# Performance work log

Measured on AMD Instinct MI355X. Metric: run time of the kernel, lower is better.

The kernel has to match this reference:

```python
import jax, jax.numpy as jnp
import numpy as np

H = 2048          # hidden_size
N = 16384         # batch (= events processed in one forward)
THR = 0.7         # event_threshold
NEG = -1e30       # masked-softmax fill


def setup_inputs() -> dict:
    key = jax.random.key(0)
    ks = jax.random.split(key, 8)
    s = lambda k, shape, scale: (jax.random.normal(k, shape, dtype=jnp.float32) * scale)
    return {
        "x": jax.random.normal(ks[0], (N, H), dtype=jnp.float32),
        "importance": jax.random.uniform(ks[1], (N,), dtype=jnp.float32),
        # event_detector: Linear(H, H//2) -> ReLU -> Linear(H//2, 1) -> Sigmoid
        "W_e1": s(ks[2], (H, H // 2), 0.02), "b_e1": jnp.zeros((H // 2,), jnp.float32),
        "W_e2": s(ks[3], (H // 2, 1), 0.05), "b_e2": jnp.ones((1,), jnp.float32),
        # retrieval_network: Linear(H, H//2) -> ReLU -> Linear(H//2, H) -> Sigmoid
        "W_r1": s(ks[4], (H, H // 2), 0.02), "b_r1": jnp.zeros((H // 2,), jnp.float32),
        "W_r2": s(ks[5], (H // 2, H), 0.02), "b_r2": jnp.zeros((H,), jnp.float32),
        "timestamp": 0,
    }


def reference(x, importance, W_e1, b_e1, W_e2, b_e2, W_r1, b_r1, W_r2, b_r2, timestamp):
    # --- detect_events: MLP -> sigmoid -> threshold -------------------------
    scores = jax.nn.sigmoid(jnp.maximum(x @ W_e1 + b_e1, 0.0) @ W_e2 + b_e2)[:, 0]  # [N]
    events = scores > THR                                   # bool mask = event-gated scatter
    has_events = jnp.any(events)

    # --- store_memory + consolidate_memories --------------------------------
    # Event rows are written into the ring buffer (no wraparound since N <= capacity);
    # consolidation = softmax over stored importances, weighted sum of stored rows.
    logits = jnp.where(events, importance, NEG)             # masked softmax over event rows
    w = jax.nn.softmax(logits)                              # [N]
    w = jnp.where(events, w, 0.0)
    consolidated = w @ x                                    # [H]

    # --- retrieve_memory -----------------------------------------------------
    # After consolidation memory_count == 1, so softmax(similarities) == 1 for
    # every query row and retrieved_memory == consolidated (broadcast to [N,H]).
    retrieved = jax.nn.sigmoid(jnp.maximum(consolidated @ W_r1 + b_r1, 0.0) @ W_r2 + b_r2)  # [H]

    # If no events fired, memory_count == 0 and retrieve_memory returns zeros.
    add = jnp.where(has_events, retrieved, jnp.zeros_like(retrieved))
    return x + add[None, :]
```

## Files before the change

### kernel.cpp

```cpp
#include <hip/hip_runtime.h>
#include <hip/hip_bf16.h>

#define H_    2048
#define NROWS 16384
#define HH    1024

typedef __bf16 bf16x8 __attribute__((ext_vector_type(8)));
typedef float  floatx4 __attribute__((ext_vector_type(4)));

__device__ __forceinline__ unsigned f2bf(float f) {
  unsigned u = __builtin_bit_cast(unsigned, f);
  u += 0x7fff + ((u >> 16) & 1);
  return u >> 16;
}

__device__ __forceinline__ void gload_lds16(const void* g, void* l) {
  __builtin_amdgcn_global_load_lds(
      (const __attribute__((address_space(1))) unsigned*)g,
      (__attribute__((address_space(3))) unsigned*)l, 16, 0, 0);
}

__global__ __launch_bounds__(256) void convert_x_kernel(
    const float* __restrict__ x, unsigned short* __restrict__ xb)
{
  size_t i = ((size_t)blockIdx.x * 256 + threadIdx.x) * 8;
  float4 v0 = *reinterpret_cast<const float4*>(x + i);
  float4 v1 = *reinterpret_cast<const float4*>(x + i + 4);
  uint4 o;
  o.x = f2bf(v0.x) | (f2bf(v0.y) << 16);
  o.y = f2bf(v0.z) | (f2bf(v0.w) << 16);
  o.z = f2bf(v1.x) | (f2bf(v1.y) << 16);
  o.w = f2bf(v1.z) | (f2bf(v1.w) << 16);
  *reinterpret_cast<uint4*>(xb + i) = o;
}

__global__ __launch_bounds__(256) void transpose_w1_kernel(
    const float* __restrict__ W1, unsigned short* __restrict__ W1t)
{
  __shared__ unsigned short tile[64][66];
  int k0 = blockIdx.x * 64;
  int n0 = blockIdx.y * 64;
  int t = threadIdx.x;
#pragma unroll
  for (int i = 0; i < 4; i++) {
    int idx = t + i * 256;
    int r = idx >> 4, c4 = (idx & 15) << 2;
    float4 v = *reinterpret_cast<const float4*>(W1 + (size_t)(k0 + r) * HH + n0 + c4);
    tile[r][c4 + 0] = (unsigned short)f2bf(v.x);
    tile[r][c4 + 1] = (unsigned short)f2bf(v.y);
    tile[r][c4 + 2] = (unsigned short)f2bf(v.z);
    tile[r][c4 + 3] = (unsigned short)f2bf(v.w);
  }
  __syncthreads();
#pragma unroll
  for (int i = 0; i < 2; i++) {
    int idx = t + i * 256;
    int n = idx >> 3, k8 = (idx & 7) << 3;
    uint4 o;
    o.x = (unsigned)tile[k8 + 0][n] | ((unsigned)tile[k8 + 1][n] << 16);
    o.y = (unsigned)tile[k8 + 2][n] | ((unsigned)tile[k8 + 3][n] << 16);
    o.z = (unsigned)tile[k8 + 4][n] | ((unsigned)tile[k8 + 5][n] << 16);
    o.w = (unsigned)tile[k8 + 6][n] | ((unsigned)tile[k8 + 7][n] << 16);
    *reinterpret_cast<uint4*>(W1t + (size_t)(n0 + n) * H_ + k0 + k8) = o;
  }
}

__global__ __launch_bounds__(256) void gemm_v2_kernel(
    const unsigned short* __restrict__ xb, const unsigned short* __restrict__ W1t,
    const float* __restrict__ b1, const float* __restrict__ W2,
    float* __restrict__ s_pre)
{
  __shared__ unsigned short As[128 * 32];
  __shared__ unsigned short Bs[128 * 32];

  const int t    = threadIdx.x;
  const int n0   = blockIdx.x * 128;
  const int m0   = blockIdx.y * 128;
  const int wave = t >> 6, lane = t & 63;
  const int wr   = (wave >> 1) * 64;
  const int wc   = (wave & 1) * 64;
  const int lcol = lane & 15, quad = lane >> 4;

  floatx4 acc[4][4] = {};

  const unsigned short* ag0 = xb  + (size_t)(m0 + (t >> 2)) * H_ + (t & 3) * 8;
  const unsigned short* ag1 = ag0 + (size_t)64 * H_;
  const unsigned short* bg0 = W1t + (size_t)(n0 + (t >> 2)) * H_ + (t & 3) * 8;
  const unsigned short* bg1 = bg0 + (size_t)64 * H_;
  unsigned short* al0 = As + 512 * wave;
  unsigned short* al1 = As + 2048 + 512 * wave;
  unsigned short* bl0 = Bs + 512 * wave;
  unsigned short* bl1 = Bs + 2048 + 512 * wave;

  for (int kk = 0; kk < H_; kk += 32) {
    __syncthreads();
    gload_lds16(ag0 + kk, al0);
    gload_lds16(ag1 + kk, al1);
    gload_lds16(bg0 + kk, bl0);
    gload_lds16(bg1 + kk, bl1);
    __syncthreads();

    bf16x8 af[4], bfr[4];
#pragma unroll
    for (int mt = 0; mt < 4; mt++)
      af[mt] = *reinterpret_cast<const bf16x8*>(As + (wr + mt * 16 + lcol) * 32 + quad * 8);
#pragma unroll
    for (int nt = 0; nt < 4; nt++)
      bfr[nt] = *reinterpret_cast<const bf16x8*>(Bs + (wc + nt * 16 + lcol) * 32 + quad * 8);
#pragma unroll
    for (int mt = 0; mt < 4; mt++)
#pragma unroll
      for (int nt = 0; nt < 4; nt++)
        acc[mt][nt] = __builtin_amdgcn_mfma_f32_16x16x32_bf16(af[mt], bfr[nt], acc[mt][nt], 0, 0, 0);
  }

  float rowsum[4][4];
#pragma unroll
  for (int mt = 0; mt < 4; mt++)
#pragma unroll
    for (int r = 0; r < 4; r++) rowsum[mt][r] = 0.f;

#pragma unroll
  for (int nt = 0; nt < 4; nt++) {
    int n = n0 + wc + nt * 16 + lcol;
    float b1v = b1[n], w2v = W2[n];
#pragma unroll
    for (int mt = 0; mt < 4; mt++)
#pragma unroll
      for (int r = 0; r < 4; r++) {
        float h = fmaxf(acc[mt][nt][r] + b1v, 0.f);
        rowsum[mt][r] = fmaf(h, w2v, rowsum[mt][r]);
      }
  }
#pragma unroll
  for (int mt = 0; mt < 4; mt++)
#pragma unroll
    for (int r = 0; r < 4; r++) {
      float s = rowsum[mt][r];
      s += __shfl_xor(s, 1); s += __shfl_xor(s, 2);
      s += __shfl_xor(s, 4); s += __shfl_xor(s, 8);
      if (lcol == 0)
        atomicAdd(&s_pre[m0 + wr + mt * 16 + quad * 4 + r], s);
    }
}

__global__ __launch_bounds__(256) void gemm_score_kernel(
    const float* __restrict__ x, const float* __restrict__ W1,
    const float* __restrict__ b1, const float* __restrict__ W2,
    float* __restrict__ s_pre)
{
  __shared__ unsigned short As[128][40];
  __shared__ unsigned short Bs[128][40];
  const int t    = threadIdx.x;
  const int n0   = blockIdx.x * 128;
  const int m0   = blockIdx.y * 128;
  const int wave = t >> 6, lane = t & 63;
  const int wr   = (wave >> 1) * 64;
  const int wc   = (wave & 1) * 64;
  const int lcol = lane & 15, quad = lane >> 4;
  floatx4 acc[4][4] = {};

  for (int kk = 0; kk < H_; kk += 32) {
    __syncthreads();
#pragma unroll
    for (int i = 0; i < 4; i++) {
      int idx = t + i * 256;
      int row = idx >> 3, k4 = (idx & 7) << 2;
      float4 v = *reinterpret_cast<const float4*>(x + (size_t)(m0 + row) * H_ + kk + k4);
      unsigned lo = f2bf(v.x) | (f2bf(v.y) << 16);
      unsigned hi = f2bf(v.z) | (f2bf(v.w) << 16);
      *reinterpret_cast<uint2*>(&As[row][k4]) = make_uint2(lo, hi);
    }
#pragma unroll
    for (int i = 0; i < 4; i++) {
      int idx = t + i * 256;
      int kr = idx >> 5, c4 = (idx & 31) << 2;
      float4 v = *reinterpret_cast<const float4*>(W1 + (size_t)(kk + kr) * HH + n0 + c4);
      Bs[c4 + 0][kr] = (unsigned short)f2bf(v.x);
      Bs[c4 + 1][kr] = (unsigned short)f2bf(v.y);
      Bs[c4 + 2][kr] = (unsigned short)f2bf(v.z);
      Bs[c4 + 3][kr] = (unsigned short)f2bf(v.w);
    }
    __syncthreads();
    bf16x8 af[4], bfr[4];
#pragma unroll
    for (int mt = 0; mt < 4; mt++)
      af[mt] = *reinterpret_cast<const bf16x8*>(&As[wr + mt * 16 + lcol][quad * 8]);
#pragma unroll
    for (int nt = 0; nt < 4; nt++)
      bfr[nt] = *reinterpret_cast<const bf16x8*>(&Bs[wc + nt * 16 + lcol][quad * 8]);
#pragma unroll
    for (int mt = 0; mt < 4; mt++)
#pragma unroll
      for (int nt = 0; nt < 4; nt++)
        acc[mt][nt] = __builtin_amdgcn_mfma_f32_16x16x32_bf16(af[mt], bfr[nt], acc[mt][nt], 0, 0, 0);
  }
  float rowsum[4][4];
#pragma unroll
  for (int mt = 0; mt < 4; mt++)
#pragma unroll
    for (int r = 0; r < 4; r++) rowsum[mt][r] = 0.f;
#pragma unroll
  for (int nt = 0; nt < 4; nt++) {
    int n = n0 + wc + nt * 16 + lcol;
    float b1v = b1[n], w2v = W2[n];
#pragma unroll
    for (int mt = 0; mt < 4; mt++)
#pragma unroll
      for (int r = 0; r < 4; r++) {
        float h = fmaxf(acc[mt][nt][r] + b1v, 0.f);
        rowsum[mt][r] = fmaf(h, w2v, rowsum[mt][r]);
      }
  }
#pragma unroll
  for (int mt = 0; mt < 4; mt++)
#pragma unroll
    for (int r = 0; r < 4; r++) {
      float s = rowsum[mt][r];
      s += __shfl_xor(s, 1); s += __shfl_xor(s, 2);
      s += __shfl_xor(s, 4); s += __shfl_xor(s, 8);
      if (lcol == 0)
        atomicAdd(&s_pre[m0 + wr + mt * 16 + quad * 4 + r], s);
    }
}

__global__ __launch_bounds__(256) void score_kernel(
    const float* __restrict__ s_pre, const float* __restrict__ imp,
    const float* __restrict__ b2, float* __restrict__ wbuf,
    float* __restrict__ Z, float* __restrict__ cnt)
{
  int i = blockIdx.x * 256 + threadIdx.x;
  float s = s_pre[i] + b2[0];
  float sig = 1.f / (1.f + __expf(-s));
  bool ev = sig > 0.7f;
  float w = ev ? __expf(imp[i]) : 0.f;
  wbuf[i] = w;
  float cw = ev ? 1.f : 0.f;
#pragma unroll
  for (int off = 32; off; off >>= 1) {
    w  += __shfl_down(w, off);
    cw += __shfl_down(cw, off);
  }
  if ((threadIdx.x & 63) == 0) {
    atomicAdd(Z, w);
    atomicAdd(cnt, cw);
  }
}

__global__ __launch_bounds__(256) void consolidate_kernel(
    const float* __restrict__ x, const float* __restrict__ wbuf,
    float* __restrict__ c)
{
  int t = threadIdx.x;
  int r0 = blockIdx.x * 128;
  float a[8] = {0.f, 0.f, 0.f, 0.f, 0.f, 0.f, 0.f, 0.f};
  for (int r = 0; r < 128; r++) {
    float w = wbuf[r0 + r];
    if (w != 0.f) {
      const float4* xr = reinterpret_cast<const float4*>(x + (size_t)(r0 + r) * H_);
      float4 v0 = xr[t], v1 = xr[t + 256];
      a[0] = fmaf(w, v0.x, a[0]); a[1] = fmaf(w, v0.y, a[1]);
      a[2] = fmaf(w, v0.z, a[2]); a[3] = fmaf(w, v0.w, a[3]);
      a[4] = fmaf(w, v1.x, a[4]); a[5] = fmaf(w, v1.y, a[5]);
      a[6] = fmaf(w, v1.z, a[6]); a[7] = fmaf(w, v1.w, a[7]);
    }
  }
  int j0 = t * 4;
  atomicAdd(&c[j0 + 0], a[0]); atomicAdd(&c[j0 + 1], a[1]);
  atomicAdd(&c[j0 + 2], a[2]); atomicAdd(&c[j0 + 3], a[3]);
  atomicAdd(&c[1024 + j0 + 0], a[4]); atomicAdd(&c[1024 + j0 + 1], a[5]);
  atomicAdd(&c[1024 + j0 + 2], a[6]); atomicAdd(&c[1024 + j0 + 3], a[7]);
}

__global__ __launch_bounds__(256) void r1_kernel(
    const float* __restrict__ c, const float* __restrict__ Z,
    const float* __restrict__ cnt, const float* __restrict__ Wr1,
    float* __restrict__ hr)
{
  __shared__ float cs[128];
  int n  = blockIdx.x * 256 + threadIdx.x;
  int k0 = blockIdx.y * 128;
  float inv = (cnt[0] > 0.5f) ? (1.f / Z[0]) : 0.f;
  if (threadIdx.x < 128) cs[threadIdx.x] = c[k0 + threadIdx.x] * inv;
  __syncthreads();
  float s = 0.f;
#pragma unroll 8
  for (int k = 0; k < 128; k++)
    s = fmaf(cs[k], Wr1[(size_t)(k0 + k) * HH + n], s);
  atomicAdd(&hr[n], s);
}

__global__ __launch_bounds__(256) void r2_kernel(
    const float* __restrict__ hr, const float* __restrict__ br1,
    const float* __restrict__ Wr2, float* __restrict__ rt)
{
  __shared__ float hs[128];
  int n  = blockIdx.x * 256 + threadIdx.x;
  int k0 = blockIdx.y * 128;
  if (threadIdx.x < 128)
    hs[threadIdx.x] = fmaxf(hr[k0 + threadIdx.x] + br1[k0 + threadIdx.x], 0.f);
  __syncthreads();
  float s = 0.f;
#pragma unroll 8
  for (int k = 0; k < 128; k++)
    s = fmaf(hs[k], Wr2[(size_t)(k0 + k) * H_ + n], s);
  atomicAdd(&rt[n], s);
}

__global__ __launch_bounds__(256) void finalize_kernel(
    const float* __restrict__ rt, const float* __restrict__ br2,
    const float* __restrict__ cnt, float* __restrict__ addv)
{
  int j = blockIdx.x * 256 + threadIdx.x;
  float v = 0.f;
  if (cnt[0] > 0.5f) v = 1.f / (1.f + expf(-(rt[j] + br2[j])));
  addv[j] = v;
}

__global__ __launch_bounds__(256) void out_kernel(
    const float* __restrict__ x, const float* __restrict__ addv,
    float* __restrict__ out)
{
  size_t i = (size_t)blockIdx.x * 256 + threadIdx.x;
  int j4 = (int)(i & 511);
  float4 a = reinterpret_cast<const float4*>(addv)[j4];
  float4 v = reinterpret_cast<const float4*>(x)[i];
  v.x += a.x; v.y += a.y; v.z += a.z; v.w += a.w;
  reinterpret_cast<float4*>(out)[i] = v;
}

extern "C" void kernel_launch(void* const* d_in, const int* in_sizes, int n_in,
                              void* d_out, int out_size, void* d_ws, size_t ws_size,
                              hipStream_t stream)
{
  (void)in_sizes; (void)n_in; (void)out_size;
  const float* x   = (const float*)d_in[0];
  const float* imp = (const float*)d_in[1];
  const float* We1 = (const float*)d_in[2];
  const float* be1 = (const float*)d_in[3];
  const float* We2 = (const float*)d_in[4];
  const float* be2 = (const float*)d_in[5];
  const float* Wr1 = (const float*)d_in[6];
  const float* br1 = (const float*)d_in[7];
  const float* Wr2 = (const float*)d_in[8];
  const float* br2 = (const float*)d_in[9];
  float* out = (float*)d_out;

  float* ws    = (float*)d_ws;
  float* s_pre = ws;
  float* c     = ws + 16384;
  float* hr    = ws + 18432;
  float* rt    = ws + 19456;
  float* Z     = ws + 21504;
  float* cnt   = ws + 21505;
  float* wbuf  = ws + 21760;
  float* addv  = ws + 38144;

  const size_t scal_bytes = 49152 * sizeof(float);
  const size_t xb_bytes   = (size_t)NROWS * H_ * 2;
  const size_t w1t_bytes  = (size_t)HH * H_ * 2;
  unsigned short* xb  = (unsigned short*)((char*)d_ws + scal_bytes);
  unsigned short* W1t = (unsigned short*)((char*)d_ws + scal_bytes + xb_bytes);
  const bool fast = ws_size >= scal_bytes + xb_bytes + w1t_bytes;

  hipMemsetAsync(d_ws, 0, 21506 * sizeof(float), stream);

  if (fast) {
    convert_x_kernel<<<16384, 256, 0, stream>>>(x, xb);
    transpose_w1_kernel<<<dim3(32, 16), 256, 0, stream>>>(We1, W1t);
    gemm_v2_kernel<<<dim3(8, 128), 256, 0, stream>>>(xb, W1t, be1, We2, s_pre);
  } else {
    gemm_score_kernel<<<dim3(8, 128), 256, 0, stream>>>(x, We1, be1, We2, s_pre);
  }
  score_kernel<<<64, 256, 0, stream>>>(s_pre, imp, be2, wbuf, Z, cnt);
  consolidate_kernel<<<128, 256, 0, stream>>>(x, wbuf, c);
  r1_kernel<<<dim3(4, 16), 256, 0, stream>>>(c, Z, cnt, Wr1, hr);
  r2_kernel<<<dim3(8, 8), 256, 0, stream>>>(hr, br1, Wr2, rt);
  finalize_kernel<<<8, 256, 0, stream>>>(rt, br2, cnt, addv);
  out_kernel<<<32768, 256, 0, stream>>>(x, addv, out);
}
```

Measured before the change: 467.8 us.

## Consolidate from bf16 copy of x, recompute weights inline, swap GEMM grid order

The consolidation pass now reads the bf16 copy of x instead of fp32, halving its memory traffic. It recomputes the event weights per block from s_pre rather than reading a stored weight buffer, and uses 512 blocks of 32 rows instead of 128 blocks of 128. The GEMM grid is transposed so consecutive blocks walk along M, which changes L2 reuse of the xb and W1t tiles. The bf16 consolidation loses precision in the weighted sum, and the old early skip of zero-weight rows is gone, so all rows are now read.

```diff
diff --git a/kernel.cpp b/kernel.cpp
--- a/kernel.cpp
+++ b/kernel.cpp
@@ -12,6 +12,12 @@
   unsigned u = __builtin_bit_cast(unsigned, f);
   u += 0x7fff + ((u >> 16) & 1);
   return u >> 16;
+}
+__device__ __forceinline__ float bflo(unsigned u) {
+  return __builtin_bit_cast(float, u << 16);
+}
+__device__ __forceinline__ float bfhi(unsigned u) {
+  return __builtin_bit_cast(float, u & 0xffff0000u);
 }
 
 __device__ __forceinline__ void gload_lds16(const void* g, void* l) {
@@ -74,8 +80,8 @@
   __shared__ unsigned short Bs[128 * 32];
 
   const int t    = threadIdx.x;
-  const int n0   = blockIdx.x * 128;
-  const int m0   = blockIdx.y * 128;
+  const int m0   = blockIdx.x * 128;
+  const int n0   = blockIdx.y * 128;
   const int wave = t >> 6, lane = t & 63;
   const int wr   = (wave >> 1) * 64;
   const int wc   = (wave & 1) * 64;
@@ -226,15 +232,13 @@
 
 __global__ __launch_bounds__(256) void score_kernel(
     const float* __restrict__ s_pre, const float* __restrict__ imp,
-    const float* __restrict__ b2, float* __restrict__ wbuf,
-    float* __restrict__ Z, float* __restrict__ cnt)
+    const float* __restrict__ b2, float* __restrict__ Z, float* __restrict__ cnt)
 {
   int i = blockIdx.x * 256 + threadIdx.x;
   float s = s_pre[i] + b2[0];
   float sig = 1.f / (1.f + __expf(-s));
   bool ev = sig > 0.7f;
   float w = ev ? __expf(imp[i]) : 0.f;
-  wbuf[i] = w;
   float cw = ev ? 1.f : 0.f;
 #pragma unroll
   for (int off = 32; off; off >>= 1) {
@@ -247,23 +251,60 @@
   }
 }
 
+__global__ __launch_bounds__(256) void consolidate_v2_kernel(
+    const unsigned short* __restrict__ xb, const float* __restrict__ s_pre,
+    const float* __restrict__ imp, const float* __restrict__ b2,
+    float* __restrict__ c)
+{
+  __shared__ float wsh[32];
+  int t = threadIdx.x;
+  int r0 = blockIdx.x * 32;
+  if (t < 32) {
+    float s = s_pre[r0 + t] + b2[0];
+    float sig = 1.f / (1.f + __expf(-s));
+    wsh[t] = (sig > 0.7f) ? __expf(imp[r0 + t]) : 0.f;
+  }
+  __syncthreads();
+  float a[8] = {0.f, 0.f, 0.f, 0.f, 0.f, 0.f, 0.f, 0.f};
+  const unsigned short* xp = xb + (size_t)r0 * H_ + t * 8;
+#pragma unroll 4
+  for (int r = 0; r < 32; r++) {
+    float w = wsh[r];
+    uint4 v = *reinterpret_cast<const uint4*>(xp + (size_t)r * H_);
+    a[0] = fmaf(w, bflo(v.x), a[0]); a[1] = fmaf(w, bfhi(v.x), a[1]);
+    a[2] = fmaf(w, bflo(v.y), a[2]); a[3] = fmaf(w, bfhi(v.y), a[3]);
+    a[4] = fmaf(w, bflo(v.z), a[4]); a[5] = fmaf(w, bfhi(v.z), a[5]);
+    a[6] = fmaf(w, bflo(v.w), a[6]); a[7] = fmaf(w, bfhi(v.w), a[7]);
+  }
+  int j0 = t * 8;
+#pragma unroll
+  for (int q = 0; q < 8; q++) atomicAdd(&c[j0 + q], a[q]);
+}
+
 __global__ __launch_bounds__(256) void consolidate_kernel(
-    const float* __restrict__ x, const float* __restrict__ wbuf,
+    const float* __restrict__ x, const float* __restrict__ s_pre,
+    const float* __restrict__ imp, const float* __restrict__ b2,
     float* __restrict__ c)
 {
+  __shared__ float wsh[32];
   int t = threadIdx.x;
-  int r0 = blockIdx.x * 128;
+  int r0 = blockIdx.x * 32;
+  if (t < 32) {
+    float s = s_pre[r0 + t] + b2[0];
+    float sig = 1.f / (1.f + __expf(-s));
+    wsh[t] = (sig > 0.7f) ? __expf(imp[r0 + t]) : 0.f;
+  }
+  __syncthreads();
   float a[8] = {0.f, 0.f, 0.f, 0.f, 0.f, 0.f, 0.f, 0.f};
-  for (int r = 0; r < 128; r++) {
-    float w = wbuf[r0 + r];
-    if (w != 0.f) {
-      const float4* xr = reinterpret_cast<const float4*>(x + (size_t)(r0 + r) * H_);
-      float4 v0 = xr[t], v1 = xr[t + 256];
-      a[0] = fmaf(w, v0.x, a[0]); a[1] = fmaf(w, v0.y, a[1]);
-      a[2] = fmaf(w, v0.z, a[2]); a[3] = fmaf(w, v0.w, a[3]);
-      a[4] = fmaf(w, v1.x, a[4]); a[5] = fmaf(w, v1.y, a[5]);
-      a[6] = fmaf(w, v1.z, a[6]); a[7] = fmaf(w, v1.w, a[7]);
-    }
+#pragma unroll 2
+  for (int r = 0; r < 32; r++) {
+    float w = wsh[r];
+    const float4* xr = reinterpret_cast<const float4*>(x + (size_t)(r0 + r) * H_);
+    float4 v0 = xr[t], v1 = xr[t + 256];
+    a[0] = fmaf(w, v0.x, a[0]); a[1] = fmaf(w, v0.y, a[1]);
+    a[2] = fmaf(w, v0.z, a[2]); a[3] = fmaf(w, v0.w, a[3]);
+    a[4] = fmaf(w, v1.x, a[4]); a[5] = fmaf(w, v1.y, a[5]);
+    a[6] = fmaf(w, v1.z, a[6]); a[7] = fmaf(w, v1.w, a[7]);
   }
   int j0 = t * 4;
   atomicAdd(&c[j0 + 0], a[0]); atomicAdd(&c[j0 + 1], a[1]);
@@ -353,7 +394,6 @@
   float* rt    = ws + 19456;
   float* Z     = ws + 21504;
   float* cnt   = ws + 21505;
-  float* wbuf  = ws + 21760;
   float* addv  = ws + 38144;
 
   const size_t scal_bytes = 49152 * sizeof(float);
@@ -368,12 +408,14 @@
   if (fast) {
     convert_x_kernel<<<16384, 256, 0, stream>>>(x, xb);
     transpose_w1_kernel<<<dim3(32, 16), 256, 0, stream>>>(We1, W1t);
-    gemm_v2_kernel<<<dim3(8, 128), 256, 0, stream>>>(xb, W1t, be1, We2, s_pre);
+    gemm_v2_kernel<<<dim3(128, 8), 256, 0, stream>>>(xb, W1t, be1, We2, s_pre);
+    score_kernel<<<64, 256, 0, stream>>>(s_pre, imp, be2, Z, cnt);
+    consolidate_v2_kernel<<<512, 256, 0, stream>>>(xb, s_pre, imp, be2, c);
   } else {
     gemm_score_kernel<<<dim3(8, 128), 256, 0, stream>>>(x, We1, be1, We2, s_pre);
-  }
-  score_kernel<<<64, 256, 0, stream>>>(s_pre, imp, be2, wbuf, Z, cnt);
-  consolidate_kernel<<<128, 256, 0, stream>>>(x, wbuf, c);
+    score_kernel<<<64, 256, 0, stream>>>(s_pre, imp, be2, Z, cnt);
+    consolidate_kernel<<<512, 256, 0, stream>>>(x, s_pre, imp, be2, c);
+  }
   r1_kernel<<<dim3(4, 16), 256, 0, stream>>>(c, Z, cnt, Wr1, hr);
   r2_kernel<<<dim3(8, 8), 256, 0, stream>>>(hr, br1, Wr2, rt);
   finalize_kernel<<<8, 256, 0, stream>>>(rt, br2, cnt, addv);
```

After: 533.1 us. +14.0%, slower.
